# Performance work log

Measured on AMD Instinct MI355X. Metric: run time of the kernel, lower is better.

Reference implementation:

```python
import jax, jax.numpy as jnp
import numpy as np

B, L, H, R = 8, 8256, 768, 24  # L = 128*129/2 flattened token-pair positions


def setup_inputs() -> dict:
    key = jax.random.key(0)
    k1, k2, k3 = jax.random.split(key, 3)
    hidden_state = jax.random.normal(k1, (B, L, H), dtype=jnp.float32)
    # per-relation Linear(hidden_size, 3) weights, stacked: (R, 3, H), (R, 3)
    W = jax.random.normal(k2, (R, 3, H), dtype=jnp.float32) * 0.02
    b = jax.random.normal(k3, (R, 3), dtype=jnp.float32) * 0.02
    return {"hidden_state": hidden_state, "W": W, "b": b}


def reference(hidden_state, W, b):
    # Batched equivalent of the per-relation Linear loop + stack(dim=1):
    # logits[b, r, l, t] = sum_h hidden_state[b,l,h] * W[r,t,h] + b[r,t]
    logits = jnp.einsum('blh,rth->brlt', hidden_state, W) + b[None, :, None, :]
    return jax.nn.softmax(logits, axis=-1)  # (B, R, L, 3)
```

## Files before the change

kernel.cpp:

```cpp
#include <hip/hip_runtime.h>
#include <hip/hip_bf16.h>


#define HD     768
#define LSEQ   8256
#define RREL   24
#define KSTEPS 24
#define NT     5
#define NCOL   72

typedef float f32x4 __attribute__((ext_vector_type(4)));
typedef short s16x8 __attribute__((ext_vector_type(8)));
typedef int   i32x4 __attribute__((ext_vector_type(4)));

__device__ __forceinline__ unsigned f2bf_rne(float f) {
  unsigned u = __builtin_bit_cast(unsigned, f);
  u += 0x7FFFu + ((u >> 16) & 1u);
  return u >> 16;
}

__device__ __forceinline__ int pack2(float lo, float hi) {
  unsigned l = __bfloat16_as_ushort(__float2bfloat16(lo));
  unsigned h = __bfloat16_as_ushort(__float2bfloat16(hi));
  return (int)(l | (h << 16));
}

__global__ void conv_w_kernel(const float* __restrict__ W,
                              unsigned short* __restrict__ wsB) {
  int idx = blockIdx.x * 256 + threadIdx.x;
  if (idx >= KSTEPS * NT * 64) return;
  int ks   = idx / (NT * 64);
  int rem  = idx - ks * (NT * 64);
  int nt   = rem >> 6;
  int lane = rem & 63;
  int col  = nt * 16 + (lane & 15);
  int k0   = ks * 32 + (lane >> 4) * 8;
  unsigned short v[8] = {0, 0, 0, 0, 0, 0, 0, 0};
  if (col < NCOL) {
    const float* p = W + (size_t)col * HD + k0;
    float4 a = *(const float4*)p;
    float4 b = *(const float4*)(p + 4);
    v[0] = (unsigned short)f2bf_rne(a.x); v[1] = (unsigned short)f2bf_rne(a.y);
    v[2] = (unsigned short)f2bf_rne(a.z); v[3] = (unsigned short)f2bf_rne(a.w);
    v[4] = (unsigned short)f2bf_rne(b.x); v[5] = (unsigned short)f2bf_rne(b.y);
    v[6] = (unsigned short)f2bf_rne(b.z); v[7] = (unsigned short)f2bf_rne(b.w);
  }
  *(s16x8*)(wsB + (size_t)idx * 8) = *(s16x8*)v;
}

#define ALOAD(ks) do { if ((ks) < KSTEPS) {                        \
    const int s_ = (ks) % 5, o_ = (ks) * 32;                       \
    abuf[s_][0][0] = *(const float4*)(pA0 + o_);                   \
    abuf[s_][0][1] = *(const float4*)(pA0 + o_ + 4);               \
    abuf[s_][1][0] = *(const float4*)(pA1 + o_);                   \
    abuf[s_][1][1] = *(const float4*)(pA1 + o_ + 4);               \
  } } while (0)

#define BLOAD_WS(ks) do { if ((ks) < KSTEPS) {                     \
    _Pragma("unroll")                                              \
    for (int nt_ = 0; nt_ < NT; ++nt_)                             \
      bbuf[(ks) % 3][nt_] = pWS[(ks) * NT * 64 + nt_ * 64 + lane]; \
  } } while (0)

#define BLOAD_FB(ks) do { if ((ks) < KSTEPS) {                     \
    _Pragma("unroll")                                              \
    for (int nt_ = 0; nt_ < 4; ++nt_) {                            \
      fbf[(ks) & 1][nt_][0] = *(const float4*)(pB[nt_] + (ks)*32); \
      fbf[(ks) & 1][nt_][1] = *(const float4*)(pB[nt_] + (ks)*32 + 4); \
    }                                                              \
    if (b4ok) {                                                    \
      fbf[(ks) & 1][4][0] = *(const float4*)(pB[4] + (ks)*32);     \
      fbf[(ks) & 1][4][1] = *(const float4*)(pB[4] + (ks)*32 + 4); \
    } else {                                                       \
      fbf[(ks) & 1][4][0] = make_float4(0.f,0.f,0.f,0.f);          \
      fbf[(ks) & 1][4][1] = make_float4(0.f,0.f,0.f,0.f);          \
    }                                                              \
  } } while (0)

template <bool USE_WS>
__global__ __launch_bounds__(64, 2)
void tagging_main(const float* __restrict__ hs, const float* __restrict__ W,
                  const float* __restrict__ bias,
                  const i32x4* __restrict__ pWS, float* __restrict__ out) {
  __shared__ float lg[32][85];

  const int lane = threadIdx.x;
  const int m0   = blockIdx.x * 32;

  const float* pA0 = hs + (size_t)(m0 + (lane >> 2)) * HD + (lane & 3) * 8;
  const float* pA1 = pA0 + 16 * HD;
  const int bp = ((lane & 15) * 4 + (lane >> 4)) * 4;

  const float* pB[NT];
  #pragma unroll
  for (int nt = 0; nt < NT; ++nt)
    pB[nt] = W + (size_t)(nt * 16 + (lane & 15)) * HD + (lane >> 4) * 8;
  const bool b4ok = (lane & 15) < 8;

  f32x4  acc[2][NT] = {};
  float4 abuf[5][2][2];
  i32x4  bbuf[3][NT];
  float4 fbf[2][NT][2];

  ALOAD(0); ALOAD(1); ALOAD(2); ALOAD(3);
  if constexpr (USE_WS) { BLOAD_WS(0); BLOAD_WS(1); } else { BLOAD_FB(0); }

  #pragma unroll
  for (int ks = 0; ks < KSTEPS; ++ks) {
    ALOAD(ks + 4);
    if constexpr (USE_WS) { BLOAD_WS(ks + 2); } else { BLOAD_FB(ks + 1); }

    s16x8 af[2];
    #pragma unroll
    for (int mt = 0; mt < 2; ++mt) {
      float4 a0 = abuf[ks % 5][mt][0], a1 = abuf[ks % 5][mt][1];
      i32x4 av;
      av[0] = __builtin_amdgcn_ds_bpermute(bp, pack2(a0.x, a0.y));
      av[1] = __builtin_amdgcn_ds_bpermute(bp, pack2(a0.z, a0.w));
      av[2] = __builtin_amdgcn_ds_bpermute(bp, pack2(a1.x, a1.y));
      av[3] = __builtin_amdgcn_ds_bpermute(bp, pack2(a1.z, a1.w));
      af[mt] = __builtin_bit_cast(s16x8, av);
    }

    #pragma unroll
    for (int nt = 0; nt < NT; ++nt) {
      s16x8 bf;
      if constexpr (USE_WS) {
        bf = __builtin_bit_cast(s16x8, bbuf[ks % 3][nt]);
      } else {
        float4 b0 = fbf[ks & 1][nt][0], b1 = fbf[ks & 1][nt][1];
        i32x4 bv;
        bv[0] = pack2(b0.x, b0.y); bv[1] = pack2(b0.z, b0.w);
        bv[2] = pack2(b1.x, b1.y); bv[3] = pack2(b1.z, b1.w);
        bf = __builtin_bit_cast(s16x8, bv);
      }
      acc[0][nt] = __builtin_amdgcn_mfma_f32_16x16x32_bf16(af[0], bf, acc[0][nt], 0, 0, 0);
      acc[1][nt] = __builtin_amdgcn_mfma_f32_16x16x32_bf16(af[1], bf, acc[1][nt], 0, 0, 0);
    }
  }

  #pragma unroll
  for (int mt = 0; mt < 2; ++mt)
    #pragma unroll
    for (int nt = 0; nt < NT; ++nt)
      #pragma unroll
      for (int j = 0; j < 4; ++j)
        lg[mt * 16 + (lane >> 4) * 4 + j][nt * 16 + (lane & 15)] = acc[mt][nt][j];
  __syncthreads();

  const int bidx = m0 / LSEQ;
  const int l0   = m0 - bidx * LSEQ;
  #pragma unroll
  for (int it = 0; it < 12; ++it) {
    int flat = it * 64 + lane;
    int g    = flat >> 5;
    int tokl = flat & 31;
    float x0 = lg[tokl][3 * g + 0] + bias[3 * g + 0];
    float x1 = lg[tokl][3 * g + 1] + bias[3 * g + 1];
    float x2 = lg[tokl][3 * g + 2] + bias[3 * g + 2];
    float mx = fmaxf(x0, fmaxf(x1, x2));
    float e0 = __expf(x0 - mx), e1 = __expf(x1 - mx), e2 = __expf(x2 - mx);
    float inv = 1.0f / (e0 + e1 + e2);
    size_t o = ((size_t)(bidx * RREL + g) * LSEQ + l0 + tokl) * 3;
    out[o + 0] = e0 * inv;
    out[o + 1] = e1 * inv;
    out[o + 2] = e2 * inv;
  }
}

extern "C" void kernel_launch(void* const* d_in, const int* in_sizes, int n_in,
                              void* d_out, int out_size, void* d_ws, size_t ws_size,
                              hipStream_t stream) {
  (void)in_sizes; (void)n_in; (void)out_size;
  const float* hs   = (const float*)d_in[0];
  const float* W    = (const float*)d_in[1];
  const float* bias = (const float*)d_in[2];
  float* out = (float*)d_out;

  const size_t needB = (size_t)KSTEPS * NT * 64 * 8 * 2;
  if (d_ws && ws_size >= needB) {
    hipLaunchKernelGGL(conv_w_kernel, dim3(30), dim3(256), 0, stream,
                       W, (unsigned short*)d_ws);
    hipLaunchKernelGGL((tagging_main<true>), dim3(2064), dim3(64), 0, stream,
                       hs, W, bias, (const i32x4*)d_ws, out);
  } else {
    hipLaunchKernelGGL((tagging_main<false>), dim3(2064), dim3(64), 0, stream,
                       hs, W, bias, nullptr, out);
  }
}
```

Before: 46.41 us.

## Stage converted weights in shared memory, shared by four waves per block

The workspace path now launches 256-thread blocks. Each of the four waves handles 32 rows, and the pre-converted bf16 weight fragments are loaded cooperatively into shared memory in two K-halves. The old path had every wave fetch all weight fragments from global or L2 on its own. The new scheme cuts that redundant traffic and the register pressure of the weight buffers. In exchange it adds block-wide barriers and 60KB of LDS per block, which may limit occupancy, and the grid shrinks to 516 blocks.

```diff
diff --git a/kernel.cpp b/kernel.cpp
--- a/kernel.cpp
+++ b/kernel.cpp
@@ -8,6 +8,8 @@
 #define KSTEPS 24
 #define NT     5
 #define NCOL   72
+#define HALFK  12
+#define CHUNKS 3840
 
 typedef float f32x4 __attribute__((ext_vector_type(4)));
 typedef short s16x8 __attribute__((ext_vector_type(8)));
@@ -56,13 +58,115 @@
     abuf[s_][1][1] = *(const float4*)(pA1 + o_ + 4);               \
   } } while (0)
 
-#define BLOAD_WS(ks) do { if ((ks) < KSTEPS) {                     \
-    _Pragma("unroll")                                              \
-    for (int nt_ = 0; nt_ < NT; ++nt_)                             \
-      bbuf[(ks) % 3][nt_] = pWS[(ks) * NT * 64 + nt_ * 64 + lane]; \
-  } } while (0)
-
-#define BLOAD_FB(ks) do { if ((ks) < KSTEPS) {                     \
+#define COMPUTE(ks, kl) do {                                        \
+    s16x8 af_[2];                                                   \
+    _Pragma("unroll")                                               \
+    for (int mt_ = 0; mt_ < 2; ++mt_) {                             \
+      float4 a0 = abuf[(ks) % 5][mt_][0], a1 = abuf[(ks) % 5][mt_][1]; \
+      i32x4 av;                                                     \
+      av[0] = __builtin_amdgcn_ds_bpermute(bp, pack2(a0.x, a0.y));  \
+      av[1] = __builtin_amdgcn_ds_bpermute(bp, pack2(a0.z, a0.w));  \
+      av[2] = __builtin_amdgcn_ds_bpermute(bp, pack2(a1.x, a1.y));  \
+      av[3] = __builtin_amdgcn_ds_bpermute(bp, pack2(a1.z, a1.w));  \
+      af_[mt_] = __builtin_bit_cast(s16x8, av);                     \
+    }                                                               \
+    _Pragma("unroll")                                               \
+    for (int nt_ = 0; nt_ < NT; ++nt_) {                            \
+      s16x8 bf_ = __builtin_bit_cast(s16x8,                         \
+          shB[((kl) * NT + nt_) * 64 + lane]);                      \
+      acc[0][nt_] = __builtin_amdgcn_mfma_f32_16x16x32_bf16(af_[0], bf_, acc[0][nt_], 0, 0, 0); \
+      acc[1][nt_] = __builtin_amdgcn_mfma_f32_16x16x32_bf16(af_[1], bf_, acc[1][nt_], 0, 0, 0); \
+    }                                                               \
+  } while (0)
+
+__global__ __launch_bounds__(256, 2)
+void tagging_ws(const float* __restrict__ hs, const float* __restrict__ bias,
+                const i32x4* __restrict__ pWS, float* __restrict__ out) {
+  __shared__ i32x4 shB[CHUNKS];
+
+  const int tid  = threadIdx.x;
+  const int lane = tid & 63;
+  const int wid  = tid >> 6;
+  const int m0   = blockIdx.x * 128 + wid * 32;
+
+  const float* pA0 = hs + (size_t)(m0 + (lane >> 2)) * HD + (lane & 3) * 8;
+  const float* pA1 = pA0 + 16 * HD;
+  const int bp = ((lane & 15) * 4 + (lane >> 4)) * 4;
+
+  f32x4  acc[2][NT] = {};
+  float4 abuf[5][2][2];
+
+  #pragma unroll
+  for (int i = 0; i < 15; ++i) shB[tid + i * 256] = pWS[tid + i * 256];
+  ALOAD(0); ALOAD(1); ALOAD(2); ALOAD(3);
+  __syncthreads();
+
+  #pragma unroll
+  for (int ks = 0; ks < HALFK; ++ks) { ALOAD(ks + 4); COMPUTE(ks, ks); }
+
+  __syncthreads();
+  #pragma unroll
+  for (int i = 0; i < 15; ++i) shB[tid + i * 256] = pWS[CHUNKS + tid + i * 256];
+  __syncthreads();
+
+  #pragma unroll
+  for (int ks = HALFK; ks < KSTEPS; ++ks) { ALOAD(ks + 4); COMPUTE(ks, ks - HALFK); }
+
+  __syncthreads();
+
+  float* lgf = (float*)shB;
+  #pragma unroll
+  for (int mt = 0; mt < 2; ++mt)
+    #pragma unroll
+    for (int nt = 0; nt < NT; ++nt)
+      #pragma unroll
+      for (int j = 0; j < 4; ++j)
+        lgf[(wid * 32 + mt * 16 + (lane >> 4) * 4 + j) * 85 + nt * 16 + (lane & 15)]
+            = acc[mt][nt][j];
+
+  const int bidx = m0 / LSEQ;
+  const int l0   = m0 - bidx * LSEQ;
+  #pragma unroll
+  for (int it = 0; it < 12; ++it) {
+    int flat = it * 64 + lane;
+    int g    = flat >> 5;
+    int tokl = flat & 31;
+    const float* row = lgf + (wid * 32 + tokl) * 85;
+    float x0 = row[3 * g + 0] + bias[3 * g + 0];
+    float x1 = row[3 * g + 1] + bias[3 * g + 1];
+    float x2 = row[3 * g + 2] + bias[3 * g + 2];
+    float mx = fmaxf(x0, fmaxf(x1, x2));
+    float e0 = __expf(x0 - mx), e1 = __expf(x1 - mx), e2 = __expf(x2 - mx);
+    float inv = 1.0f / (e0 + e1 + e2);
+    size_t o = ((size_t)(bidx * RREL + g) * LSEQ + l0 + tokl) * 3;
+    out[o + 0] = e0 * inv;
+    out[o + 1] = e1 * inv;
+    out[o + 2] = e2 * inv;
+  }
+}
+
+__global__ __launch_bounds__(64, 2)
+void tagging_fb(const float* __restrict__ hs, const float* __restrict__ W,
+                const float* __restrict__ bias, float* __restrict__ out) {
+  __shared__ float lg[32][85];
+  const int lane = threadIdx.x;
+  const int m0   = blockIdx.x * 32;
+
+  const float* pA0 = hs + (size_t)(m0 + (lane >> 2)) * HD + (lane & 3) * 8;
+  const float* pA1 = pA0 + 16 * HD;
+  const int bp = ((lane & 15) * 4 + (lane >> 4)) * 4;
+
+  const float* pB[NT];
+  #pragma unroll
+  for (int nt = 0; nt < NT; ++nt)
+    pB[nt] = W + (size_t)(nt * 16 + (lane & 15)) * HD + (lane >> 4) * 8;
+  const bool b4ok = (lane & 15) < 8;
+
+  f32x4  acc[2][NT] = {};
+  float4 abuf[5][2][2];
+  float4 fbf[2][NT][2];
+
+#define FB_BLOAD(ks) do { if ((ks) < KSTEPS) {                     \
     _Pragma("unroll")                                              \
     for (int nt_ = 0; nt_ < 4; ++nt_) {                            \
       fbf[(ks) & 1][nt_][0] = *(const float4*)(pB[nt_] + (ks)*32); \
@@ -77,39 +181,13 @@
     }                                                              \
   } } while (0)
 
-template <bool USE_WS>
-__global__ __launch_bounds__(64, 2)
-void tagging_main(const float* __restrict__ hs, const float* __restrict__ W,
-                  const float* __restrict__ bias,
-                  const i32x4* __restrict__ pWS, float* __restrict__ out) {
-  __shared__ float lg[32][85];
-
-  const int lane = threadIdx.x;
-  const int m0   = blockIdx.x * 32;
-
-  const float* pA0 = hs + (size_t)(m0 + (lane >> 2)) * HD + (lane & 3) * 8;
-  const float* pA1 = pA0 + 16 * HD;
-  const int bp = ((lane & 15) * 4 + (lane >> 4)) * 4;
-
-  const float* pB[NT];
-  #pragma unroll
-  for (int nt = 0; nt < NT; ++nt)
-    pB[nt] = W + (size_t)(nt * 16 + (lane & 15)) * HD + (lane >> 4) * 8;
-  const bool b4ok = (lane & 15) < 8;
-
-  f32x4  acc[2][NT] = {};
-  float4 abuf[5][2][2];
-  i32x4  bbuf[3][NT];
-  float4 fbf[2][NT][2];
-
   ALOAD(0); ALOAD(1); ALOAD(2); ALOAD(3);
-  if constexpr (USE_WS) { BLOAD_WS(0); BLOAD_WS(1); } else { BLOAD_FB(0); }
+  FB_BLOAD(0);
 
   #pragma unroll
   for (int ks = 0; ks < KSTEPS; ++ks) {
     ALOAD(ks + 4);
-    if constexpr (USE_WS) { BLOAD_WS(ks + 2); } else { BLOAD_FB(ks + 1); }
-
+    FB_BLOAD(ks + 1);
     s16x8 af[2];
     #pragma unroll
     for (int mt = 0; mt < 2; ++mt) {
@@ -121,19 +199,13 @@
       av[3] = __builtin_amdgcn_ds_bpermute(bp, pack2(a1.z, a1.w));
       af[mt] = __builtin_bit_cast(s16x8, av);
     }
-
     #pragma unroll
     for (int nt = 0; nt < NT; ++nt) {
-      s16x8 bf;
-      if constexpr (USE_WS) {
-        bf = __builtin_bit_cast(s16x8, bbuf[ks % 3][nt]);
-      } else {
-        float4 b0 = fbf[ks & 1][nt][0], b1 = fbf[ks & 1][nt][1];
-        i32x4 bv;
-        bv[0] = pack2(b0.x, b0.y); bv[1] = pack2(b0.z, b0.w);
-        bv[2] = pack2(b1.x, b1.y); bv[3] = pack2(b1.z, b1.w);
-        bf = __builtin_bit_cast(s16x8, bv);
-      }
+      float4 b0 = fbf[ks & 1][nt][0], b1 = fbf[ks & 1][nt][1];
+      i32x4 bv;
+      bv[0] = pack2(b0.x, b0.y); bv[1] = pack2(b0.z, b0.w);
+      bv[2] = pack2(b1.x, b1.y); bv[3] = pack2(b1.z, b1.w);
+      s16x8 bf = __builtin_bit_cast(s16x8, bv);
       acc[0][nt] = __builtin_amdgcn_mfma_f32_16x16x32_bf16(af[0], bf, acc[0][nt], 0, 0, 0);
       acc[1][nt] = __builtin_amdgcn_mfma_f32_16x16x32_bf16(af[1], bf, acc[1][nt], 0, 0, 0);
     }
@@ -181,10 +253,10 @@
   if (d_ws && ws_size >= needB) {
     hipLaunchKernelGGL(conv_w_kernel, dim3(30), dim3(256), 0, stream,
                        W, (unsigned short*)d_ws);
-    hipLaunchKernelGGL((tagging_main<true>), dim3(2064), dim3(64), 0, stream,
-                       hs, W, bias, (const i32x4*)d_ws, out);
+    hipLaunchKernelGGL(tagging_ws, dim3(516), dim3(256), 0, stream,
+                       hs, bias, (const i32x4*)d_ws, out);
   } else {
-    hipLaunchKernelGGL((tagging_main<false>), dim3(2064), dim3(64), 0, stream,
-                       hs, W, bias, nullptr, out);
-  }
-}
+    hipLaunchKernelGGL(tagging_fb, dim3(2064), dim3(64), 0, stream,
+                       hs, W, bias, out);
+  }
+}
```

New measurement: 54.42 us. 17.3% more time.
